# Kernel optimization log

Hardware: AMD Instinct MI355X
Metric: run time of the kernel (lower is better)

The kernel has to match this reference:

```python
import jax, jax.numpy as jnp
import numpy as np
from jax import lax

B, T, MEL, D, H, NC = 8, 256, 128, 192, 4, 20
C_EVENT, C_SCENE = 8, 64
ETA, LR, ALPHA = 0.9, 0.1, 0.01  # memory momentum, write lr, forget rate
EPS = 1e-5


def _ln(x, g, b):
    m = x.mean(-1, keepdims=True)
    v = ((x - m) ** 2).mean(-1, keepdims=True)
    return (x - m) / jnp.sqrt(v + EPS) * g + b


def _mem_step(x, t, M, S, Wk, Wv, Wq, chunk):
    # x: [B,D]; M,S: [B,D,D]. Titans-style neural memory, updated every `chunk` steps.
    k = x @ Wk
    v = x @ Wv
    q = x @ Wq
    err = v - jnp.einsum('bd,bde->be', k, M)          # surprise / prediction error
    S_new = ETA * S + LR * jnp.einsum('bd,be->bde', k, err)
    M_new = (1.0 - ALPHA) * M + S_new
    upd = (t % chunk) == 0
    S = jnp.where(upd, S_new, S)
    M = jnp.where(upd, M_new, M)
    out = jnp.einsum('bd,bde->be', q, M)              # retrieval
    return out, M, S


def setup_inputs() -> dict:
    key = jax.random.key(0)
    ks = jax.random.split(key, 24)
    w = lambda k, shp, s=0.05: jax.random.normal(k, shp, dtype=jnp.float32) * s
    inp = {
        'x': jax.random.normal(ks[0], (B, T, MEL), dtype=jnp.float32),
        'W_in': w(ks[1], (MEL, D)), 'b_in': jnp.zeros((D,), jnp.float32),
        # MHA at seq_len=1: softmax over one key -> weight 1, so only V and out proj matter
        'Wv_a': w(ks[2], (D, D)), 'bv_a': jnp.zeros((D,), jnp.float32),
        'Wo_a': w(ks[3], (D, D)), 'bo_a': jnp.zeros((D,), jnp.float32),
        # conformer conv module (degenerate seq_len=1: depthwise conv -> center tap)
        'ln1_g': jnp.ones((D,), jnp.float32), 'ln1_b': jnp.zeros((D,), jnp.float32),
        'pw1_w': w(ks[4], (D, 2 * D)), 'pw1_b': jnp.zeros((2 * D,), jnp.float32),
        'dw_w': w(ks[5], (D,), 0.2), 'dw_b': jnp.zeros((D,), jnp.float32),
        'bn_s': jnp.ones((D,), jnp.float32), 'bn_b': jnp.zeros((D,), jnp.float32),
        'pw2_w': w(ks[6], (D, D)), 'pw2_b': jnp.zeros((D,), jnp.float32),
        # theta (event) / delta (scene) neural memory projections
        'Wk_t': w(ks[7], (D, D)), 'Wv_t': w(ks[8], (D, D)), 'Wq_t': w(ks[9], (D, D)),
        'Wk_d': w(ks[10], (D, D)), 'Wv_d': w(ks[11], (D, D)), 'Wq_d': w(ks[12], (D, D)),
        'ln2_g': jnp.ones((D,), jnp.float32), 'ln2_b': jnp.zeros((D,), jnp.float32),
        'Wc': w(ks[13], (D, NC)), 'bc': jnp.zeros((NC,), jnp.float32),
    }
    return inp


def reference(x, W_in, b_in, Wv_a, bv_a, Wo_a, bo_a, ln1_g, ln1_b, pw1_w, pw1_b,
              dw_w, dw_b, bn_s, bn_b, pw2_w, pw2_b, Wk_t, Wv_t, Wq_t,
              Wk_d, Wv_d, Wq_d, ln2_g, ln2_b, Wc, bc):
    xp = x @ W_in + b_in                               # [B,T,D]

    def step(carry, inp):
        x_t, t = inp                                   # x_t: [B,D]
        Mt, St, Md, Sd = carry
        d_out, Md, Sd = _mem_step(x_t, t, Md, Sd, Wk_d, Wv_d, Wq_d, C_SCENE)
        x1 = x_t + 0.5 * d_out
        attn = (x1 @ Wv_a + bv_a) @ Wo_a + bo_a        # single-token self-attn
        x2 = x1 + attn
        h = _ln(x2, ln1_g, ln1_b)
        h = h @ pw1_w + pw1_b
        a, g = jnp.split(h, 2, axis=-1)
        h = a * jax.nn.sigmoid(g)                      # GLU
        h = h * dw_w + dw_b                            # depthwise conv center tap
        h = h * bn_s + bn_b                            # eval-mode BN
        h = jax.nn.silu(h)
        h = h @ pw2_w + pw2_b
        x3 = x2 + h
        t_out, Mt, St = _mem_step(x3, t, Mt, St, Wk_t, Wv_t, Wq_t, C_EVENT)
        x4 = x3 + 0.5 * t_out
        return (Mt, St, Md, Sd), _ln(x4, ln2_g, ln2_b)

    z = jnp.zeros((B, D, D), jnp.float32)
    xs = (jnp.swapaxes(xp, 0, 1), jnp.arange(T))       # [T,B,D], [T]
    _, ys = lax.scan(step, (z, z, z, z), xs)
    y = jnp.swapaxes(ys, 0, 1)                         # [B,T,D]
    pooled = y.mean(axis=1)
    return pooled @ Wc + bc                            # [B,NC]
```

## Files before the change

### kernel.cpp

```cpp
#include <hip/hip_runtime.h>
#include <math.h>

#define Bb 8
#define Tt 256
#define MEL 128
#define Dd 192
#define NCc 20
#define ND 4
#define NT 32
#define ETAc 0.9f
#define LRc 0.1f
#define MDEC 0.99f
#define EPSc 1e-5f
#define PT 4
#define RTT 8
#define PADD 196
#define UPAD 193

__device__ __forceinline__ float sigmoidf_(float x) {
    return 1.0f / (1.0f + __expf(-x));
}

__device__ __forceinline__ float memcoef(int n, int i) {
    float m = LRc, pw = LRc;
    for (int nn = i + 1; nn <= n; nn++) { pw *= ETAc; m = MDEC * m + pw; }
    return m;
}

__device__ __forceinline__ float dot4(float4 a, float4 b) {
    return a.x * b.x + a.y * b.y + a.z * b.z + a.w * b.w;
}

__global__ __launch_bounds__(192) void setup(
    const float* __restrict__ Wv_a, const float* __restrict__ Wo_a,
    const float* __restrict__ bv_a, const float* __restrict__ bo_a,
    const float* __restrict__ Wq_t, const float* __restrict__ Wq_d,
    const float* __restrict__ x, const float* __restrict__ W_in,
    const float* __restrict__ b_in, const float* __restrict__ Wk_d,
    const float* __restrict__ Wv_d,
    float* __restrict__ Wavo_ws, float* __restrict__ b_avo,
    float* __restrict__ WqtT, float* __restrict__ WqdT,
    float* __restrict__ Kd_ws, float* __restrict__ Vd_ws,
    float* __restrict__ pooled, unsigned int* __restrict__ ctr)
{
    __shared__ __align__(16) float smem[512];
    int blk = blockIdx.x, tid = threadIdx.x;

    if (blk < 192) {
        int m = blk;
        smem[tid] = Wv_a[m * Dd + tid];
        __syncthreads();
        int o = tid;
        float acc = 0.f;
        #pragma unroll 8
        for (int k = 0; k < Dd; k += 4) {
            acc += Wo_a[(k + 0) * Dd + o] * smem[k + 0];
            acc += Wo_a[(k + 1) * Dd + o] * smem[k + 1];
            acc += Wo_a[(k + 2) * Dd + o] * smem[k + 2];
            acc += Wo_a[(k + 3) * Dd + o] * smem[k + 3];
        }
        Wavo_ws[m * Dd + o] = acc;
        return;
    }
    if (blk == 192) {
        int o = tid;
        float s = bo_a[o];
        #pragma unroll 4
        for (int m = 0; m < Dd; m++) s += bv_a[m] * Wo_a[m * Dd + o];
        b_avo[o] = s;
        return;
    }
    if (blk < 241) {
        int r0 = 4 * (blk - 193);
        float4 v;
        v.x = Wq_t[(r0 + 0) * Dd + tid];
        v.y = Wq_t[(r0 + 1) * Dd + tid];
        v.z = Wq_t[(r0 + 2) * Dd + tid];
        v.w = Wq_t[(r0 + 3) * Dd + tid];
        *(float4*)&WqtT[tid * Dd + r0] = v;
        return;
    }
    if (blk < 289) {
        int r0 = 4 * (blk - 241);
        float4 v;
        v.x = Wq_d[(r0 + 0) * Dd + tid];
        v.y = Wq_d[(r0 + 1) * Dd + tid];
        v.z = Wq_d[(r0 + 2) * Dd + tid];
        v.w = Wq_d[(r0 + 3) * Dd + tid];
        *(float4*)&WqdT[tid * Dd + r0] = v;
        return;
    }
    if (blk == 289) {
        for (int q = tid; q < Bb * Dd; q += 192) pooled[q] = 0.f;
        if (tid == 0) *ctr = 0u;
        return;
    }

    int q = blk - 290;
    int b = q >> 2, i = q & 3;
    float* XR = smem;
    float* XP = smem + 128;
    if (tid < 128) XR[tid] = x[((size_t)b * Tt + 64 * i) * MEL + tid];
    __syncthreads();
    {
        int o = tid;
        float acc = b_in[o];
        #pragma unroll 8
        for (int k = 0; k < MEL; k += 4) {
            acc += W_in[(k + 0) * Dd + o] * XR[k + 0];
            acc += W_in[(k + 1) * Dd + o] * XR[k + 1];
            acc += W_in[(k + 2) * Dd + o] * XR[k + 2];
            acc += W_in[(k + 3) * Dd + o] * XR[k + 3];
        }
        XP[o] = acc;
    }
    __syncthreads();
    {
        int o = tid;
        float ak = 0.f, av = 0.f;
        #pragma unroll 4
        for (int k = 0; k < Dd; k += 4) {
            float x0 = XP[k + 0], x1 = XP[k + 1], x2 = XP[k + 2], x3 = XP[k + 3];
            ak += Wk_d[(k + 0) * Dd + o] * x0 + Wk_d[(k + 1) * Dd + o] * x1
                + Wk_d[(k + 2) * Dd + o] * x2 + Wk_d[(k + 3) * Dd + o] * x3;
            av += Wv_d[(k + 0) * Dd + o] * x0 + Wv_d[(k + 1) * Dd + o] * x1
                + Wv_d[(k + 2) * Dd + o] * x2 + Wv_d[(k + 3) * Dd + o] * x3;
        }
        Kd_ws[(b * ND + i) * Dd + o] = ak;
        Vd_ws[(b * ND + i) * Dd + o] = av;
    }
}

__global__ __launch_bounds__(192) void delta_solve(
    const float* __restrict__ WqdT, const float* __restrict__ Kd_ws,
    float* __restrict__ Vd_ws, float* __restrict__ Ud_ws)
{
    int blk = blockIdx.x, b = blk / 5, role = blk % 5, tid = threadIdx.x;
    if (role == 0) {
        __shared__ __align__(16) float K4[ND][Dd], V4[ND][Dd];
        __shared__ float G[16], mc[16];
        for (int q = tid; q < ND * 48; q += 192) {
            int i = q / 48, c = q - i * 48;
            ((float4*)K4[i])[c] = ((const float4*)&Kd_ws[(b * ND + i) * Dd])[c];
            ((float4*)V4[i])[c] = ((const float4*)&Vd_ws[(b * ND + i) * Dd])[c];
        }
        __syncthreads();
        if (tid < 16) {
            int i = tid >> 2, j = tid & 3;
            float s = 0.f;
            for (int d = 0; d < Dd; d++) s += K4[i][d] * K4[j][d];
            G[tid] = s;
            mc[tid] = (j <= i) ? memcoef(i, j) : 0.f;
        }
        __syncthreads();
        for (int i = 1; i < ND; i++) {
            float acc = V4[i][tid];
            for (int m = 0; m < i; m++)
                acc -= mc[(i - 1) * ND + m] * G[i * ND + m] * V4[m][tid];
            V4[i][tid] = acc;
        }
        for (int i = 0; i < ND; i++) Vd_ws[(b * ND + i) * Dd + tid] = V4[i][tid];
    } else {
        __shared__ float KS[Dd];
        int i = role - 1;
        KS[tid] = Kd_ws[(b * ND + i) * Dd + tid];
        __syncthreads();
        int o = tid;
        float acc = 0.f;
        #pragma unroll 8
        for (int k = 0; k < Dd; k += 4) {
            acc += WqdT[(k + 0) * Dd + o] * KS[k + 0];
            acc += WqdT[(k + 1) * Dd + o] * KS[k + 1];
            acc += WqdT[(k + 2) * Dd + o] * KS[k + 2];
            acc += WqdT[(k + 3) * Dd + o] * KS[k + 3];
        }
        Ud_ws[(b * ND + i) * Dd + o] = acc;
    }
}

__global__ __launch_bounds__(192) void pipeline(
    const float* __restrict__ x, const float* __restrict__ W_in,
    const float* __restrict__ b_in,
    const float* __restrict__ ln1_g, const float* __restrict__ ln1_b,
    const float* __restrict__ pw1_w, const float* __restrict__ pw1_b,
    const float* __restrict__ dw_w, const float* __restrict__ dw_b,
    const float* __restrict__ bn_s, const float* __restrict__ bn_b,
    const float* __restrict__ pw2_w, const float* __restrict__ pw2_b,
    const float* __restrict__ Wavo_ws, const float* __restrict__ b_avo,
    const float* __restrict__ Ed_ws, const float* __restrict__ Ud_ws,
    const float* __restrict__ Wk_t, const float* __restrict__ Wv_t,
    const float* __restrict__ WqtT,
    float* __restrict__ x3_ws, float* __restrict__ Kt_ws,
    float* __restrict__ Vt_ws, float* __restrict__ Ut_ws)
{
    int blk = blockIdx.x;
    int b = blk >> 6, tile = blk & 63;
    int t0 = tile * PT, n = tile >> 4;
    int tid = threadIdx.x;

    __shared__ __align__(16) float XR[PT][MEL];
    __shared__ __align__(16) float XP[PT][Dd];
    __shared__ __align__(16) float ED[ND][PADD], UD[ND][PADD];
    __shared__ __align__(16) float X1[PT][Dd], X2[PT][Dd];
    __shared__ __align__(16) float LNX[PT][Dd], HG[PT][Dd];
    __shared__ float X3row[Dd];
    __shared__ float KTs[Dd];
    __shared__ float WQs[PT * ND];
    __shared__ float mv[PT][2];

    if (tid < 128) {
        int r = tid >> 5, c = tid & 31;
        ((float4*)XR[r])[c] = ((const float4*)&x[((size_t)b * Tt + t0 + r) * MEL])[c];
    }
    for (int q = tid; q < ND * 48 * 2; q += 192) {
        int which = q >= ND * 48;
        int qq = which ? q - ND * 48 : q;
        int i = qq / 48, c = qq - i * 48;
        if (!which) ((float4*)ED[i])[c] = ((const float4*)&Ed_ws[(b * ND + i) * Dd])[c];
        else        ((float4*)UD[i])[c] = ((const float4*)&Ud_ws[(b * ND + i) * Dd])[c];
    }
    __syncthreads();

    int o = tid;
    {
        float acc[PT];
        float bb = b_in[o];
        #pragma unroll
        for (int r = 0; r < PT; r++) acc[r] = bb;
        #pragma unroll 8
        for (int k = 0; k < MEL; k += 4) {
            float w0 = W_in[(k + 0) * Dd + o], w1 = W_in[(k + 1) * Dd + o];
            float w2 = W_in[(k + 2) * Dd + o], w3 = W_in[(k + 3) * Dd + o];
            #pragma unroll
            for (int r = 0; r < PT; r++) {
                float4 xv = *(const float4*)&XR[r][k];
                acc[r] += w0 * xv.x + w1 * xv.y + w2 * xv.z + w3 * xv.w;
            }
        }
        #pragma unroll
        for (int r = 0; r < PT; r++) XP[r][tid] = acc[r];
    }
    __syncthreads();

    if (tid < 128) {
        int r = tid >> 5, i = (tid >> 3) & 3, c = tid & 7;
        float s = 0.f;
        const float* xp = XP[r];
        const float* u = UD[i];
        #pragma unroll
        for (int j = 0; j < 24; j++) s += xp[c * 24 + j] * u[c * 24 + j];
        s += __shfl_down(s, 4, 8);
        s += __shfl_down(s, 2, 8);
        s += __shfl_down(s, 1, 8);
        if (c == 0) {
            float coef = (i <= n) ? memcoef(n, i) : 0.f;
            WQs[r * ND + i] = s * coef;
        }
    }
    __syncthreads();

    {
        #pragma unroll
        for (int r = 0; r < PT; r++) {
            float dout = WQs[r * ND + 0] * ED[0][tid] + WQs[r * ND + 1] * ED[1][tid]
                       + WQs[r * ND + 2] * ED[2][tid] + WQs[r * ND + 3] * ED[3][tid];
            X1[r][tid] = XP[r][tid] + 0.5f * dout;
        }
    }
    __syncthreads();

    {
        float acc[PT];
        float bb = b_avo[o];
        #pragma unroll
        for (int r = 0; r < PT; r++) acc[r] = bb;
        #pragma unroll 8
        for (int k = 0; k < Dd; k += 4) {
            float w0 = Wavo_ws[(k + 0) * Dd + o], w1 = Wavo_ws[(k + 1) * Dd + o];
            float w2 = Wavo_ws[(k + 2) * Dd + o], w3 = Wavo_ws[(k + 3) * Dd + o];
            #pragma unroll
            for (int r = 0; r < PT; r++) {
                float4 xv = *(const float4*)&X1[r][k];
                acc[r] += w0 * xv.x + w1 * xv.y + w2 * xv.z + w3 * xv.w;
            }
        }
        #pragma unroll
        for (int r = 0; r < PT; r++) X2[r][tid] = X1[r][tid] + acc[r];
    }
    __syncthreads();

    if (tid < 128) {
        int r = tid >> 5, j = tid & 31;
        float s = 0.f, sq = 0.f;
        for (int d = j; d < Dd; d += 32) { float v = X2[r][d]; s += v; sq += v * v; }
        for (int off = 16; off > 0; off >>= 1) {
            s += __shfl_down(s, off, 32); sq += __shfl_down(sq, off, 32);
        }
        if (j == 0) {
            float mean = s / Dd;
            mv[r][0] = mean;
            mv[r][1] = rsqrtf(sq / Dd - mean * mean + EPSc);
        }
    }
    __syncthreads();
    {
        float g = ln1_g[tid], bb = ln1_b[tid];
        #pragma unroll
        for (int r = 0; r < PT; r++)
            LNX[r][tid] = (X2[r][tid] - mv[r][0]) * mv[r][1] * g + bb;
    }
    __syncthreads();

    {
        float aa[PT], gg[PT];
        float ba = pw1_b[o], bg = pw1_b[o + Dd];
        #pragma unroll
        for (int r = 0; r < PT; r++) { aa[r] = ba; gg[r] = bg; }
        #pragma unroll 4
        for (int k = 0; k < Dd; k += 4) {
            float wa0 = pw1_w[(k + 0) * 2 * Dd + o], wg0 = pw1_w[(k + 0) * 2 * Dd + Dd + o];
            float wa1 = pw1_w[(k + 1) * 2 * Dd + o], wg1 = pw1_w[(k + 1) * 2 * Dd + Dd + o];
            float wa2 = pw1_w[(k + 2) * 2 * Dd + o], wg2 = pw1_w[(k + 2) * 2 * Dd + Dd + o];
            float wa3 = pw1_w[(k + 3) * 2 * Dd + o], wg3 = pw1_w[(k + 3) * 2 * Dd + Dd + o];
            #pragma unroll
            for (int r = 0; r < PT; r++) {
                float4 xv = *(const float4*)&LNX[r][k];
                aa[r] += wa0 * xv.x + wa1 * xv.y + wa2 * xv.z + wa3 * xv.w;
                gg[r] += wg0 * xv.x + wg1 * xv.y + wg2 * xv.z + wg3 * xv.w;
            }
        }
        float dww = dw_w[o], dwb = dw_b[o], bns = bn_s[o], bnb = bn_b[o];
        #pragma unroll
        for (int r = 0; r < PT; r++) {
            float h = aa[r] * sigmoidf_(gg[r]);
            h = h * dww + dwb;
            h = h * bns + bnb;
            h = h * sigmoidf_(h);
            HG[r][tid] = h;
        }
    }
    __syncthreads();

    {
        float acc[PT];
        float bb = pw2_b[o];
        #pragma unroll
        for (int r = 0; r < PT; r++) acc[r] = bb;
        #pragma unroll 8
        for (int k = 0; k < Dd; k += 4) {
            float w0 = pw2_w[(k + 0) * Dd + o], w1 = pw2_w[(k + 1) * Dd + o];
            float w2 = pw2_w[(k + 2) * Dd + o], w3 = pw2_w[(k + 3) * Dd + o];
            #pragma unroll
            for (int r = 0; r < PT; r++) {
                float4 xv = *(const float4*)&HG[r][k];
                acc[r] += w0 * xv.x + w1 * xv.y + w2 * xv.z + w3 * xv.w;
            }
        }
        #pragma unroll
        for (int r = 0; r < PT; r++) {
            float v = X2[r][tid] + acc[r];
            if (r == 0) X3row[tid] = v;
            x3_ws[((size_t)b * Tt + t0 + r) * Dd + tid] = v;
        }
    }

    if ((tile & 1) == 0) {
        int i8 = tile >> 1;
        __syncthreads();
        {
            float ak = 0.f, av = 0.f;
            #pragma unroll 4
            for (int k = 0; k < Dd; k += 4) {
                float x0 = X3row[k + 0], x1v = X3row[k + 1];
                float x2v = X3row[k + 2], x3v = X3row[k + 3];
                ak += Wk_t[(k + 0) * Dd + o] * x0 + Wk_t[(k + 1) * Dd + o] * x1v
                    + Wk_t[(k + 2) * Dd + o] * x2v + Wk_t[(k + 3) * Dd + o] * x3v;
                av += Wv_t[(k + 0) * Dd + o] * x0 + Wv_t[(k + 1) * Dd + o] * x1v
                    + Wv_t[(k + 2) * Dd + o] * x2v + Wv_t[(k + 3) * Dd + o] * x3v;
            }
            Kt_ws[(b * NT + i8) * Dd + o] = ak;
            Vt_ws[(b * NT + i8) * Dd + o] = av;
            KTs[o] = ak;
        }
        __syncthreads();
        {
            float au = 0.f;
            #pragma unroll 8
            for (int k = 0; k < Dd; k += 4) {
                au += WqtT[(k + 0) * Dd + o] * KTs[k + 0]
                    + WqtT[(k + 1) * Dd + o] * KTs[k + 1]
                    + WqtT[(k + 2) * Dd + o] * KTs[k + 2]
                    + WqtT[(k + 3) * Dd + o] * KTs[k + 3];
            }
            Ut_ws[(b * NT + i8) * Dd + o] = au;
        }
    }
}

__global__ __launch_bounds__(192) void theta_solve(
    const float* __restrict__ Kt_ws, const float* __restrict__ Vt_ws,
    float* __restrict__ Et_ws)
{
    int b = blockIdx.x, tid = threadIdx.x;
    __shared__ __align__(16) float K[NT][PADD], V[NT][PADD];
    __shared__ float G[NT * NT], mcc[NT * NT];
    __shared__ float T[NT * 33];

    for (int q = tid; q < NT * 48; q += 192) {
        int i = q / 48, c = q - i * 48;
        ((float4*)K[i])[c] = ((const float4*)&Kt_ws[(b * NT + i) * Dd])[c];
        ((float4*)V[i])[c] = ((const float4*)&Vt_ws[(b * NT + i) * Dd])[c];
    }
    if (tid < NT) {
        int i = tid;
        float m = 0.f, pw = LRc;
        for (int nn = 0; nn < NT; nn++) {
            float v;
            if (nn < i) v = 0.f;
            else if (nn == i) { m = LRc; v = m; }
            else { pw *= ETAc; m = MDEC * m + pw; v = m; }
            mcc[nn * NT + i] = v;
        }
    }
    __syncthreads();
    for (int p = tid; p < NT * NT; p += 192) {
        int i = p >> 5, j = p & 31;
        const float4* ki = (const float4*)K[i];
        const float4* kj = (const float4*)K[j];
        float s = 0.f;
        #pragma unroll 4
        for (int kk = 0; kk < 48; kk++) s += dot4(ki[kk], kj[kk]);
        G[p] = s;
    }
    __syncthreads();
    for (int p = tid; p < NT * NT; p += 192) {
        int i = p >> 5, m = p & 31;
        G[p] = (m < i) ? mcc[(i - 1) * NT + m] * G[p] : 0.f;
    }
    __syncthreads();
    if (tid < NT) {
        int j = tid;
        T[j * 33 + j] = 1.f;
        for (int i = j + 1; i < NT; i++) {
            float s = 0.f;
            for (int m = j; m < i; m++) s += G[i * NT + m] * T[m * 33 + j];
            T[i * 33 + j] = -s;
        }
    }
    __syncthreads();
    {
        for (int i = 0; i < NT; i++) {
            float s = 0.f;
            for (int j = 0; j <= i; j++) s += T[i * 33 + j] * V[j][tid];
            Et_ws[(b * NT + i) * Dd + tid] = s;
        }
    }
}

__global__ __launch_bounds__(256) void retrieve(
    const float* __restrict__ x3_ws, const float* __restrict__ Ut_ws,
    const float* __restrict__ Et_ws, const float* __restrict__ ln2_g,
    const float* __restrict__ ln2_b, float* __restrict__ pooled,
    const float* __restrict__ Wc, const float* __restrict__ bc,
    float* __restrict__ out, unsigned int* __restrict__ ctr)
{
    int blk = blockIdx.x, b = blk >> 5, tile = blk & 31;
    int t0 = tile * RTT, n = tile;
    int tid = threadIdx.x;

    __shared__ float UT[NT][UPAD];
    __shared__ __align__(16) float XS[RTT][PADD];
    __shared__ float WQ[RTT * NT];
    __shared__ float mv[RTT][2];
    __shared__ float PLD[Bb * Dd];
    __shared__ bool isLast;

    for (int q = tid; q < NT * Dd; q += 256) {
        int i = q / Dd, c = q - i * Dd;
        UT[i][c] = Ut_ws[(size_t)b * NT * Dd + q];
    }
    for (int q = tid; q < RTT * 48; q += 256) {
        int r = q / 48, c = q - r * 48;
        ((float4*)XS[r])[c] = ((const float4*)&x3_ws[((size_t)b * Tt + t0 + r) * Dd])[c];
    }
    __syncthreads();

    {
        int r = tid >> 5, i = tid & 31;
        const float* u = UT[i];
        const float* xr = XS[r];
        float s = 0.f;
        #pragma unroll 8
        for (int kk = 0; kk < Dd; kk++) s += u[kk] * xr[kk];
        float coef = (i <= n) ? memcoef(n, i) : 0.f;
        WQ[tid] = s * coef;
    }
    __syncthreads();

    if (tid < Dd) {
        float acc[RTT] = {};
        #pragma unroll 4
        for (int i = 0; i < NT; i++) {
            float e = Et_ws[(b * NT + i) * Dd + tid];
            #pragma unroll
            for (int r = 0; r < RTT; r++) acc[r] += WQ[r * NT + i] * e;
        }
        #pragma unroll
        for (int r = 0; r < RTT; r++) XS[r][tid] += 0.5f * acc[r];
    }
    __syncthreads();

    {
        int r = tid >> 5, j = tid & 31;
        float s = 0.f, sq = 0.f;
        for (int d = j; d < Dd; d += 32) { float v = XS[r][d]; s += v; sq += v * v; }
        for (int off = 16; off > 0; off >>= 1) {
            s += __shfl_down(s, off, 32); sq += __shfl_down(sq, off, 32);
        }
        if (j == 0) {
            float mean = s / Dd;
            mv[r][0] = mean;
            mv[r][1] = rsqrtf(sq / Dd - mean * mean + EPSc);
        }
    }
    __syncthreads();

    if (tid < Dd) {
        float g = ln2_g[tid], bb = ln2_b[tid];
        float sum = 0.f;
        #pragma unroll
        for (int r = 0; r < RTT; r++)
            sum += (XS[r][tid] - mv[r][0]) * mv[r][1] * g + bb;
        atomicAdd(&pooled[b * Dd + tid], sum);
    }

    __threadfence();
    if (tid == 0) {
        unsigned int old = atomicAdd(ctr, 1u);
        isLast = (old == (unsigned)(Bb * 32 - 1));
    }
    __syncthreads();
    if (isLast) {
        __threadfence();
        for (int q = tid; q < Bb * Dd; q += 256)
            PLD[q] = *(volatile const float*)&pooled[q];
        __syncthreads();
        if (tid < Bb * NCc) {
            int bo = tid / NCc, c = tid - bo * NCc;
            float s = 0.f;
            for (int d = 0; d < Dd; d++) s += PLD[bo * Dd + d] * Wc[d * NCc + c];
            out[tid] = s * (1.0f / Tt) + bc[c];
        }
    }
}

extern "C" void kernel_launch(void* const* d_in, const int* in_sizes, int n_in,
                              void* d_out, int out_size, void* d_ws, size_t ws_size,
                              hipStream_t stream) {
    const float* x     = (const float*)d_in[0];
    const float* W_in  = (const float*)d_in[1];
    const float* b_in  = (const float*)d_in[2];
    const float* Wv_a  = (const float*)d_in[3];
    const float* bv_a  = (const float*)d_in[4];
    const float* Wo_a  = (const float*)d_in[5];
    const float* bo_a  = (const float*)d_in[6];
    const float* ln1_g = (const float*)d_in[7];
    const float* ln1_b = (const float*)d_in[8];
    const float* pw1_w = (const float*)d_in[9];
    const float* pw1_b = (const float*)d_in[10];
    const float* dw_w  = (const float*)d_in[11];
    const float* dw_b  = (const float*)d_in[12];
    const float* bn_s  = (const float*)d_in[13];
    const float* bn_b  = (const float*)d_in[14];
    const float* pw2_w = (const float*)d_in[15];
    const float* pw2_b = (const float*)d_in[16];
    const float* Wk_t  = (const float*)d_in[17];
    const float* Wv_t  = (const float*)d_in[18];
    const float* Wq_t  = (const float*)d_in[19];
    const float* Wk_d  = (const float*)d_in[20];
    const float* Wv_d  = (const float*)d_in[21];
    const float* Wq_d  = (const float*)d_in[22];
    const float* ln2_g = (const float*)d_in[23];
    const float* ln2_b = (const float*)d_in[24];
    const float* Wc    = (const float*)d_in[25];
    const float* bc    = (const float*)d_in[26];

    float* ws = (float*)d_ws;
    size_t off = 0;
    float* x3_ws   = ws + off; off += (size_t)Bb * Tt * Dd;
    float* Kd_ws   = ws + off; off += Bb * ND * Dd;
    float* Vd_ws   = ws + off; off += Bb * ND * Dd;
    float* Ud_ws   = ws + off; off += Bb * ND * Dd;
    float* Kt_ws   = ws + off; off += Bb * NT * Dd;
    float* Vt_ws   = ws + off; off += Bb * NT * Dd;
    float* Et_ws   = ws + off; off += Bb * NT * Dd;
    float* Ut_ws   = ws + off; off += Bb * NT * Dd;
    float* pooled  = ws + off; off += Bb * Dd;
    float* Wavo_ws = ws + off; off += Dd * Dd;
    float* WqtT    = ws + off; off += Dd * Dd;
    float* WqdT    = ws + off; off += Dd * Dd;
    float* b_avo   = ws + off; off += Dd;
    unsigned int* ctr = (unsigned int*)(ws + off); off += 1;

    setup<<<322, 192, 0, stream>>>(
        Wv_a, Wo_a, bv_a, bo_a, Wq_t, Wq_d,
        x, W_in, b_in, Wk_d, Wv_d,
        Wavo_ws, b_avo, WqtT, WqdT, Kd_ws, Vd_ws, pooled, ctr);
    delta_solve<<<Bb * 5, 192, 0, stream>>>(WqdT, Kd_ws, Vd_ws, Ud_ws);
    pipeline<<<Bb * 64, 192, 0, stream>>>(
        x, W_in, b_in, ln1_g, ln1_b, pw1_w, pw1_b, dw_w, dw_b,
        bn_s, bn_b, pw2_w, pw2_b, Wavo_ws, b_avo, Vd_ws, Ud_ws,
        Wk_t, Wv_t, WqtT, x3_ws, Kt_ws, Vt_ws, Ut_ws);
    theta_solve<<<Bb, 192, 0, stream>>>(Kt_ws, Vt_ws, Et_ws);
    retrieve<<<Bb * 32, 256, 0, stream>>>(
        x3_ws, Ut_ws, Et_ws, ln2_g, ln2_b, pooled, Wc, bc, (float*)d_out, ctr);
}
```

Baseline: 224.7 us.

## Fuse all stages into one cooperative persistent kernel with grid syncs

Replaces the five separate kernel launches with a single cooperative kernel that runs each phase in a grid-stride loop, separated by grid.sync(). The pipeline is also split into finer phases (separate theta-solve stages and a final classifier phase), all sharing one LDS union. The aim is to remove launch gaps and the atomic last-block counter. In exchange it adds grid-wide barrier costs, forces a 256-thread block shape where only 192 threads work in many phases, and reduces occupancy because the LDS union is sized for the largest phase.

```diff
diff --git a/kernel.cpp b/kernel.cpp
--- a/kernel.cpp
+++ b/kernel.cpp
@@ -1,5 +1,8 @@
 #include <hip/hip_runtime.h>
+#include <hip/hip_cooperative_groups.h>
 #include <math.h>
+
+namespace cg = cooperative_groups;
 
 #define Bb 8
 #define Tt 256
@@ -16,6 +19,13 @@
 #define RTT 8
 #define PADD 196
 #define UPAD 193
+#define BLK_THR 256
+#define NA 322
+#define NB 40
+#define NC_ 512
+#define NDp 256
+#define NE 8
+#define NF 256
 
 __device__ __forceinline__ float sigmoidf_(float x) {
     return 1.0f / (1.0f + __expf(-x));
@@ -31,222 +41,211 @@
     return a.x * b.x + a.y * b.y + a.z * b.z + a.w * b.w;
 }
 
-__global__ __launch_bounds__(192) void setup(
-    const float* __restrict__ Wv_a, const float* __restrict__ Wo_a,
-    const float* __restrict__ bv_a, const float* __restrict__ bo_a,
-    const float* __restrict__ Wq_t, const float* __restrict__ Wq_d,
-    const float* __restrict__ x, const float* __restrict__ W_in,
-    const float* __restrict__ b_in, const float* __restrict__ Wk_d,
-    const float* __restrict__ Wv_d,
-    float* __restrict__ Wavo_ws, float* __restrict__ b_avo,
-    float* __restrict__ WqtT, float* __restrict__ WqdT,
-    float* __restrict__ Kd_ws, float* __restrict__ Vd_ws,
-    float* __restrict__ pooled, unsigned int* __restrict__ ctr)
-{
-    __shared__ __align__(16) float smem[512];
-    int blk = blockIdx.x, tid = threadIdx.x;
-
+struct CoopArgs {
+    const float *x, *W_in, *b_in, *Wv_a, *bv_a, *Wo_a, *bo_a;
+    const float *ln1_g, *ln1_b, *pw1_w, *pw1_b, *dw_w, *dw_b, *bn_s, *bn_b;
+    const float *pw2_w, *pw2_b, *Wk_t, *Wv_t, *Wq_t, *Wk_d, *Wv_d, *Wq_d;
+    const float *ln2_g, *ln2_b, *Wc, *bc;
+    float *x3_ws, *Kd_ws, *Vd_ws, *Ud_ws, *Kt_ws, *Vt_ws, *Et_ws, *Ut_ws;
+    float *Sg_ws, *pooled, *Wavo_ws, *WqtT, *WqdT, *b_avo, *out;
+};
+
+struct LdsA { float col[Dd]; float XR[MEL]; float XP[Dd]; };
+struct LdsB { float K4[ND][Dd]; float V4[ND][Dd]; float G[16], mc[16]; float KS[Dd]; };
+struct LdsC {
+    float XR[PT][MEL]; float XP[PT][Dd];
+    float ED[ND][PADD], UD[ND][PADD];
+    float X1[PT][Dd], X2[PT][Dd], LNX[PT][Dd], HG[PT][Dd];
+    float WQs[PT * ND]; float mv[PT][2];
+};
+struct LdsD { float XS[Dd]; float KS[Dd]; };
+struct LdsE1 { float K[NT][PADD]; };
+struct LdsE2 { float S[NT * NT]; float T[NT * 33]; };
+struct LdsF { float UT[NT][UPAD]; float XS[RTT][PADD]; float WQ[RTT * NT]; float mv[RTT][2]; };
+struct LdsG { float PLD[Bb * Dd]; };
+
+union LDSU {
+    LdsA a; LdsB b; LdsC c; LdsD d; LdsE1 e1; LdsE2 e2; LdsF f; LdsG g;
+};
+
+__device__ void phaseA(const CoopArgs& a, LdsA& L, int blk, int tid)
+{
     if (blk < 192) {
         int m = blk;
-        smem[tid] = Wv_a[m * Dd + tid];
+        if (tid < Dd) L.col[tid] = a.Wv_a[m * Dd + tid];
         __syncthreads();
-        int o = tid;
-        float acc = 0.f;
-        #pragma unroll 8
-        for (int k = 0; k < Dd; k += 4) {
-            acc += Wo_a[(k + 0) * Dd + o] * smem[k + 0];
-            acc += Wo_a[(k + 1) * Dd + o] * smem[k + 1];
-            acc += Wo_a[(k + 2) * Dd + o] * smem[k + 2];
-            acc += Wo_a[(k + 3) * Dd + o] * smem[k + 3];
-        }
-        Wavo_ws[m * Dd + o] = acc;
-        return;
-    }
-    if (blk == 192) {
-        int o = tid;
-        float s = bo_a[o];
-        #pragma unroll 4
-        for (int m = 0; m < Dd; m++) s += bv_a[m] * Wo_a[m * Dd + o];
-        b_avo[o] = s;
-        return;
-    }
-    if (blk < 241) {
+        if (tid < Dd) {
+            int o = tid;
+            float acc = 0.f;
+            #pragma unroll 8
+            for (int k = 0; k < Dd; k += 4) {
+                acc += a.Wo_a[(k + 0) * Dd + o] * L.col[k + 0];
+                acc += a.Wo_a[(k + 1) * Dd + o] * L.col[k + 1];
+                acc += a.Wo_a[(k + 2) * Dd + o] * L.col[k + 2];
+                acc += a.Wo_a[(k + 3) * Dd + o] * L.col[k + 3];
+            }
+            a.Wavo_ws[m * Dd + o] = acc;
+        }
+    } else if (blk == 192) {
+        if (tid < Dd) {
+            int o = tid;
+            float s = a.bo_a[o];
+            #pragma unroll 4
+            for (int m = 0; m < Dd; m++) s += a.bv_a[m] * a.Wo_a[m * Dd + o];
+            a.b_avo[o] = s;
+        }
+    } else if (blk < 241) {
         int r0 = 4 * (blk - 193);
-        float4 v;
-        v.x = Wq_t[(r0 + 0) * Dd + tid];
-        v.y = Wq_t[(r0 + 1) * Dd + tid];
-        v.z = Wq_t[(r0 + 2) * Dd + tid];
-        v.w = Wq_t[(r0 + 3) * Dd + tid];
-        *(float4*)&WqtT[tid * Dd + r0] = v;
-        return;
-    }
-    if (blk < 289) {
+        if (tid < Dd) {
+            float4 v;
+            v.x = a.Wq_t[(r0 + 0) * Dd + tid];
+            v.y = a.Wq_t[(r0 + 1) * Dd + tid];
+            v.z = a.Wq_t[(r0 + 2) * Dd + tid];
+            v.w = a.Wq_t[(r0 + 3) * Dd + tid];
+            *(float4*)&a.WqtT[tid * Dd + r0] = v;
+        }
+    } else if (blk < 289) {
         int r0 = 4 * (blk - 241);
-        float4 v;
-        v.x = Wq_d[(r0 + 0) * Dd + tid];
-        v.y = Wq_d[(r0 + 1) * Dd + tid];
-        v.z = Wq_d[(r0 + 2) * Dd + tid];
-        v.w = Wq_d[(r0 + 3) * Dd + tid];
-        *(float4*)&WqdT[tid * Dd + r0] = v;
-        return;
-    }
-    if (blk == 289) {
-        for (int q = tid; q < Bb * Dd; q += 192) pooled[q] = 0.f;
-        if (tid == 0) *ctr = 0u;
-        return;
-    }
-
-    int q = blk - 290;
-    int b = q >> 2, i = q & 3;
-    float* XR = smem;
-    float* XP = smem + 128;
-    if (tid < 128) XR[tid] = x[((size_t)b * Tt + 64 * i) * MEL + tid];
-    __syncthreads();
-    {
-        int o = tid;
-        float acc = b_in[o];
-        #pragma unroll 8
-        for (int k = 0; k < MEL; k += 4) {
-            acc += W_in[(k + 0) * Dd + o] * XR[k + 0];
-            acc += W_in[(k + 1) * Dd + o] * XR[k + 1];
-            acc += W_in[(k + 2) * Dd + o] * XR[k + 2];
-            acc += W_in[(k + 3) * Dd + o] * XR[k + 3];
-        }
-        XP[o] = acc;
-    }
-    __syncthreads();
-    {
-        int o = tid;
-        float ak = 0.f, av = 0.f;
-        #pragma unroll 4
-        for (int k = 0; k < Dd; k += 4) {
-            float x0 = XP[k + 0], x1 = XP[k + 1], x2 = XP[k + 2], x3 = XP[k + 3];
-            ak += Wk_d[(k + 0) * Dd + o] * x0 + Wk_d[(k + 1) * Dd + o] * x1
-                + Wk_d[(k + 2) * Dd + o] * x2 + Wk_d[(k + 3) * Dd + o] * x3;
-            av += Wv_d[(k + 0) * Dd + o] * x0 + Wv_d[(k + 1) * Dd + o] * x1
-                + Wv_d[(k + 2) * Dd + o] * x2 + Wv_d[(k + 3) * Dd + o] * x3;
-        }
-        Kd_ws[(b * ND + i) * Dd + o] = ak;
-        Vd_ws[(b * ND + i) * Dd + o] = av;
-    }
-}
-
-__global__ __launch_bounds__(192) void delta_solve(
-    const float* __restrict__ WqdT, const float* __restrict__ Kd_ws,
-    float* __restrict__ Vd_ws, float* __restrict__ Ud_ws)
-{
-    int blk = blockIdx.x, b = blk / 5, role = blk % 5, tid = threadIdx.x;
+        if (tid < Dd) {
+            float4 v;
+            v.x = a.Wq_d[(r0 + 0) * Dd + tid];
+            v.y = a.Wq_d[(r0 + 1) * Dd + tid];
+            v.z = a.Wq_d[(r0 + 2) * Dd + tid];
+            v.w = a.Wq_d[(r0 + 3) * Dd + tid];
+            *(float4*)&a.WqdT[tid * Dd + r0] = v;
+        }
+    } else if (blk == 289) {
+        for (int q = tid; q < Bb * Dd; q += BLK_THR) a.pooled[q] = 0.f;
+    } else if (blk < 322) {
+        int q = blk - 290;
+        int b = q >> 2, i = q & 3;
+        if (tid < 128) L.XR[tid] = a.x[((size_t)b * Tt + 64 * i) * MEL + tid];
+        __syncthreads();
+        if (tid < Dd) {
+            int o = tid;
+            float acc = a.b_in[o];
+            #pragma unroll 8
+            for (int k = 0; k < MEL; k += 4) {
+                acc += a.W_in[(k + 0) * Dd + o] * L.XR[k + 0];
+                acc += a.W_in[(k + 1) * Dd + o] * L.XR[k + 1];
+                acc += a.W_in[(k + 2) * Dd + o] * L.XR[k + 2];
+                acc += a.W_in[(k + 3) * Dd + o] * L.XR[k + 3];
+            }
+            L.XP[o] = acc;
+        }
+        __syncthreads();
+        if (tid < Dd) {
+            int o = tid;
+            float ak = 0.f, av = 0.f;
+            #pragma unroll 4
+            for (int k = 0; k < Dd; k += 4) {
+                float x0 = L.XP[k + 0], x1 = L.XP[k + 1];
+                float x2 = L.XP[k + 2], x3 = L.XP[k + 3];
+                ak += a.Wk_d[(k + 0) * Dd + o] * x0 + a.Wk_d[(k + 1) * Dd + o] * x1
+                    + a.Wk_d[(k + 2) * Dd + o] * x2 + a.Wk_d[(k + 3) * Dd + o] * x3;
+                av += a.Wv_d[(k + 0) * Dd + o] * x0 + a.Wv_d[(k + 1) * Dd + o] * x1
+                    + a.Wv_d[(k + 2) * Dd + o] * x2 + a.Wv_d[(k + 3) * Dd + o] * x3;
+            }
+            a.Kd_ws[(b * ND + i) * Dd + o] = ak;
+            a.Vd_ws[(b * ND + i) * Dd + o] = av;
+        }
+    }
+    __syncthreads();
+}
+
+__device__ void phaseB(const CoopArgs& a, LdsB& L, int blk, int tid)
+{
+    int b = blk / 5, role = blk % 5;
     if (role == 0) {
-        __shared__ __align__(16) float K4[ND][Dd], V4[ND][Dd];
-        __shared__ float G[16], mc[16];
-        for (int q = tid; q < ND * 48; q += 192) {
-            int i = q / 48, c = q - i * 48;
-            ((float4*)K4[i])[c] = ((const float4*)&Kd_ws[(b * ND + i) * Dd])[c];
-            ((float4*)V4[i])[c] = ((const float4*)&Vd_ws[(b * ND + i) * Dd])[c];
+        for (int q = tid; q < ND * Dd; q += BLK_THR) {
+            int i = q / Dd, c = q - i * Dd;
+            L.K4[i][c] = a.Kd_ws[(size_t)b * ND * Dd + q];
+            L.V4[i][c] = a.Vd_ws[(size_t)b * ND * Dd + q];
         }
         __syncthreads();
         if (tid < 16) {
             int i = tid >> 2, j = tid & 3;
             float s = 0.f;
-            for (int d = 0; d < Dd; d++) s += K4[i][d] * K4[j][d];
-            G[tid] = s;
-            mc[tid] = (j <= i) ? memcoef(i, j) : 0.f;
+            for (int d = 0; d < Dd; d++) s += L.K4[i][d] * L.K4[j][d];
+            L.G[tid] = s;
+            L.mc[tid] = (j <= i) ? memcoef(i, j) : 0.f;
         }
         __syncthreads();
-        for (int i = 1; i < ND; i++) {
-            float acc = V4[i][tid];
-            for (int m = 0; m < i; m++)
-                acc -= mc[(i - 1) * ND + m] * G[i * ND + m] * V4[m][tid];
-            V4[i][tid] = acc;
-        }
-        for (int i = 0; i < ND; i++) Vd_ws[(b * ND + i) * Dd + tid] = V4[i][tid];
+        if (tid < Dd) {
+            for (int i = 1; i < ND; i++) {
+                float acc = L.V4[i][tid];
+                for (int m = 0; m < i; m++)
+                    acc -= L.mc[(i - 1) * ND + m] * L.G[i * ND + m] * L.V4[m][tid];
+                L.V4[i][tid] = acc;
+            }
+            for (int i = 0; i < ND; i++)
+                a.Vd_ws[(b * ND + i) * Dd + tid] = L.V4[i][tid];
+        }
     } else {
-        __shared__ float KS[Dd];
         int i = role - 1;
-        KS[tid] = Kd_ws[(b * ND + i) * Dd + tid];
+        if (tid < Dd) L.KS[tid] = a.Kd_ws[(b * ND + i) * Dd + tid];
         __syncthreads();
-        int o = tid;
-        float acc = 0.f;
-        #pragma unroll 8
-        for (int k = 0; k < Dd; k += 4) {
-            acc += WqdT[(k + 0) * Dd + o] * KS[k + 0];
-            acc += WqdT[(k + 1) * Dd + o] * KS[k + 1];
-            acc += WqdT[(k + 2) * Dd + o] * KS[k + 2];
-            acc += WqdT[(k + 3) * Dd + o] * KS[k + 3];
-        }
-        Ud_ws[(b * ND + i) * Dd + o] = acc;
-    }
-}
-
-__global__ __launch_bounds__(192) void pipeline(
-    const float* __restrict__ x, const float* __restrict__ W_in,
-    const float* __restrict__ b_in,
-    const float* __restrict__ ln1_g, const float* __restrict__ ln1_b,
-    const float* __restrict__ pw1_w, const float* __restrict__ pw1_b,
-    const float* __restrict__ dw_w, const float* __restrict__ dw_b,
-    const float* __restrict__ bn_s, const float* __restrict__ bn_b,
-    const float* __restrict__ pw2_w, const float* __restrict__ pw2_b,
-    const float* __restrict__ Wavo_ws, const float* __restrict__ b_avo,
-    const float* __restrict__ Ed_ws, const float* __restrict__ Ud_ws,
-    const float* __restrict__ Wk_t, const float* __restrict__ Wv_t,
-    const float* __restrict__ WqtT,
-    float* __restrict__ x3_ws, float* __restrict__ Kt_ws,
-    float* __restrict__ Vt_ws, float* __restrict__ Ut_ws)
-{
-    int blk = blockIdx.x;
+        if (tid < Dd) {
+            int o = tid;
+            float acc = 0.f;
+            #pragma unroll 8
+            for (int k = 0; k < Dd; k += 4) {
+                acc += a.WqdT[(k + 0) * Dd + o] * L.KS[k + 0];
+                acc += a.WqdT[(k + 1) * Dd + o] * L.KS[k + 1];
+                acc += a.WqdT[(k + 2) * Dd + o] * L.KS[k + 2];
+                acc += a.WqdT[(k + 3) * Dd + o] * L.KS[k + 3];
+            }
+            a.Ud_ws[(b * ND + i) * Dd + o] = acc;
+        }
+    }
+    __syncthreads();
+}
+
+__device__ void phaseC(const CoopArgs& a, LdsC& L, int blk, int tid)
+{
     int b = blk >> 6, tile = blk & 63;
     int t0 = tile * PT, n = tile >> 4;
-    int tid = threadIdx.x;
-
-    __shared__ __align__(16) float XR[PT][MEL];
-    __shared__ __align__(16) float XP[PT][Dd];
-    __shared__ __align__(16) float ED[ND][PADD], UD[ND][PADD];
-    __shared__ __align__(16) float X1[PT][Dd], X2[PT][Dd];
-    __shared__ __align__(16) float LNX[PT][Dd], HG[PT][Dd];
-    __shared__ float X3row[Dd];
-    __shared__ float KTs[Dd];
-    __shared__ float WQs[PT * ND];
-    __shared__ float mv[PT][2];
 
     if (tid < 128) {
         int r = tid >> 5, c = tid & 31;
-        ((float4*)XR[r])[c] = ((const float4*)&x[((size_t)b * Tt + t0 + r) * MEL])[c];
-    }
-    for (int q = tid; q < ND * 48 * 2; q += 192) {
+        ((float4*)L.XR[r])[c] =
+            ((const float4*)&a.x[((size_t)b * Tt + t0 + r) * MEL])[c];
+    }
+    for (int q = tid; q < ND * 48 * 2; q += BLK_THR) {
         int which = q >= ND * 48;
         int qq = which ? q - ND * 48 : q;
         int i = qq / 48, c = qq - i * 48;
-        if (!which) ((float4*)ED[i])[c] = ((const float4*)&Ed_ws[(b * ND + i) * Dd])[c];
-        else        ((float4*)UD[i])[c] = ((const float4*)&Ud_ws[(b * ND + i) * Dd])[c];
+        if (!which) ((float4*)L.ED[i])[c] = ((const float4*)&a.Vd_ws[(b * ND + i) * Dd])[c];
+        else        ((float4*)L.UD[i])[c] = ((const float4*)&a.Ud_ws[(b * ND + i) * Dd])[c];
     }
     __syncthreads();
 
     int o = tid;
-    {
+    if (tid < Dd) {
         float acc[PT];
-        float bb = b_in[o];
+        float bb = a.b_in[o];
         #pragma unroll
         for (int r = 0; r < PT; r++) acc[r] = bb;
         #pragma unroll 8
         for (int k = 0; k < MEL; k += 4) {
-            float w0 = W_in[(k + 0) * Dd + o], w1 = W_in[(k + 1) * Dd + o];
-            float w2 = W_in[(k + 2) * Dd + o], w3 = W_in[(k + 3) * Dd + o];
+            float w0 = a.W_in[(k + 0) * Dd + o], w1 = a.W_in[(k + 1) * Dd + o];
+            float w2 = a.W_in[(k + 2) * Dd + o], w3 = a.W_in[(k + 3) * Dd + o];
             #pragma unroll
             for (int r = 0; r < PT; r++) {
-                float4 xv = *(const float4*)&XR[r][k];
+                float4 xv = *(const float4*)&L.XR[r][k];
                 acc[r] += w0 * xv.x + w1 * xv.y + w2 * xv.z + w3 * xv.w;
             }
         }
         #pragma unroll
-        for (int r = 0; r < PT; r++) XP[r][tid] = acc[r];
+        for (int r = 0; r < PT; r++) L.XP[r][tid] = acc[r];
     }
     __syncthreads();
 
     if (tid < 128) {
         int r = tid >> 5, i = (tid >> 3) & 3, c = tid & 7;
         float s = 0.f;
-        const float* xp = XP[r];
-        const float* u = UD[i];
+        const float* xp = L.XP[r];
+        const float* u = L.UD[i];
         #pragma unroll
         for (int j = 0; j < 24; j++) s += xp[c * 24 + j] * u[c * 24 + j];
         s += __shfl_down(s, 4, 8);
@@ -254,246 +253,236 @@
         s += __shfl_down(s, 1, 8);
         if (c == 0) {
             float coef = (i <= n) ? memcoef(n, i) : 0.f;
-            WQs[r * ND + i] = s * coef;
-        }
-    }
-    __syncthreads();
-
-    {
+            L.WQs[r * ND + i] = s * coef;
+        }
+    }
+    __syncthreads();
+
+    if (tid < Dd) {
         #pragma unroll
         for (int r = 0; r < PT; r++) {
-            float dout = WQs[r * ND + 0] * ED[0][tid] + WQs[r * ND + 1] * ED[1][tid]
-                       + WQs[r * ND + 2] * ED[2][tid] + WQs[r * ND + 3] * ED[3][tid];
-            X1[r][tid] = XP[r][tid] + 0.5f * dout;
-        }
-    }
-    __syncthreads();
-
-    {
+            float dout = L.WQs[r * ND + 0] * L.ED[0][tid]
+                       + L.WQs[r * ND + 1] * L.ED[1][tid]
+                       + L.WQs[r * ND + 2] * L.ED[2][tid]
+                       + L.WQs[r * ND + 3] * L.ED[3][tid];
+            L.X1[r][tid] = L.XP[r][tid] + 0.5f * dout;
+        }
+    }
+    __syncthreads();
+
+    if (tid < Dd) {
         float acc[PT];
-        float bb = b_avo[o];
+        float bb = a.b_avo[o];
         #pragma unroll
         for (int r = 0; r < PT; r++) acc[r] = bb;
         #pragma unroll 8
         for (int k = 0; k < Dd; k += 4) {
-            float w0 = Wavo_ws[(k + 0) * Dd + o], w1 = Wavo_ws[(k + 1) * Dd + o];
-            float w2 = Wavo_ws[(k + 2) * Dd + o], w3 = Wavo_ws[(k + 3) * Dd + o];
+            float w0 = a.Wavo_ws[(k + 0) * Dd + o], w1 = a.Wavo_ws[(k + 1) * Dd + o];
+            float w2 = a.Wavo_ws[(k + 2) * Dd + o], w3 = a.Wavo_ws[(k + 3) * Dd + o];
             #pragma unroll
             for (int r = 0; r < PT; r++) {
-                float4 xv = *(const float4*)&X1[r][k];
+                float4 xv = *(const float4*)&L.X1[r][k];
                 acc[r] += w0 * xv.x + w1 * xv.y + w2 * xv.z + w3 * xv.w;
             }
         }
         #pragma unroll
-        for (int r = 0; r < PT; r++) X2[r][tid] = X1[r][tid] + acc[r];
+        for (int r = 0; r < PT; r++) L.X2[r][tid] = L.X1[r][tid] + acc[r];
     }
     __syncthreads();
 
     if (tid < 128) {
         int r = tid >> 5, j = tid & 31;
         float s = 0.f, sq = 0.f;
-        for (int d = j; d < Dd; d += 32) { float v = X2[r][d]; s += v; sq += v * v; }
+        for (int d = j; d < Dd; d += 32) { float v = L.X2[r][d]; s += v; sq += v * v; }
         for (int off = 16; off > 0; off >>= 1) {
             s += __shfl_down(s, off, 32); sq += __shfl_down(sq, off, 32);
         }
         if (j == 0) {
             float mean = s / Dd;
-            mv[r][0] = mean;
-            mv[r][1] = rsqrtf(sq / Dd - mean * mean + EPSc);
-        }
-    }
-    __syncthreads();
-    {
-        float g = ln1_g[tid], bb = ln1_b[tid];
+            L.mv[r][0] = mean;
+            L.mv[r][1] = rsqrtf(sq / Dd - mean * mean + EPSc);
+        }
+    }
+    __syncthreads();
+    if (tid < Dd) {
+        float g = a.ln1_g[tid], bb = a.ln1_b[tid];
         #pragma unroll
         for (int r = 0; r < PT; r++)
-            LNX[r][tid] = (X2[r][tid] - mv[r][0]) * mv[r][1] * g + bb;
-    }
-    __syncthreads();
-
-    {
+            L.LNX[r][tid] = (L.X2[r][tid] - L.mv[r][0]) * L.mv[r][1] * g + bb;
+    }
+    __syncthreads();
+
+    if (tid < Dd) {
         float aa[PT], gg[PT];
-        float ba = pw1_b[o], bg = pw1_b[o + Dd];
+        float ba = a.pw1_b[o], bg = a.pw1_b[o + Dd];
         #pragma unroll
         for (int r = 0; r < PT; r++) { aa[r] = ba; gg[r] = bg; }
         #pragma unroll 4
         for (int k = 0; k < Dd; k += 4) {
-            float wa0 = pw1_w[(k + 0) * 2 * Dd + o], wg0 = pw1_w[(k + 0) * 2 * Dd + Dd + o];
-            float wa1 = pw1_w[(k + 1) * 2 * Dd + o], wg1 = pw1_w[(k + 1) * 2 * Dd + Dd + o];
-            float wa2 = pw1_w[(k + 2) * 2 * Dd + o], wg2 = pw1_w[(k + 2) * 2 * Dd + Dd + o];
-            float wa3 = pw1_w[(k + 3) * 2 * Dd + o], wg3 = pw1_w[(k + 3) * 2 * Dd + Dd + o];
+            float wa0 = a.pw1_w[(k + 0) * 2 * Dd + o], wg0 = a.pw1_w[(k + 0) * 2 * Dd + Dd + o];
+            float wa1 = a.pw1_w[(k + 1) * 2 * Dd + o], wg1 = a.pw1_w[(k + 1) * 2 * Dd + Dd + o];
+            float wa2 = a.pw1_w[(k + 2) * 2 * Dd + o], wg2 = a.pw1_w[(k + 2) * 2 * Dd + Dd + o];
+            float wa3 = a.pw1_w[(k + 3) * 2 * Dd + o], wg3 = a.pw1_w[(k + 3) * 2 * Dd + Dd + o];
             #pragma unroll
             for (int r = 0; r < PT; r++) {
-                float4 xv = *(const float4*)&LNX[r][k];
+                float4 xv = *(const float4*)&L.LNX[r][k];
                 aa[r] += wa0 * xv.x + wa1 * xv.y + wa2 * xv.z + wa3 * xv.w;
                 gg[r] += wg0 * xv.x + wg1 * xv.y + wg2 * xv.z + wg3 * xv.w;
             }
         }
-        float dww = dw_w[o], dwb = dw_b[o], bns = bn_s[o], bnb = bn_b[o];
+        float dww = a.dw_w[o], dwb = a.dw_b[o], bns = a.bn_s[o], bnb = a.bn_b[o];
         #pragma unroll
         for (int r = 0; r < PT; r++) {
             float h = aa[r] * sigmoidf_(gg[r]);
             h = h * dww + dwb;
             h = h * bns + bnb;
             h = h * sigmoidf_(h);
-            HG[r][tid] = h;
-        }
-    }
-    __syncthreads();
-
-    {
+            L.HG[r][tid] = h;
+        }
+    }
+    __syncthreads();
+
+    if (tid < Dd) {
         float acc[PT];
-        float bb = pw2_b[o];
+        float bb = a.pw2_b[o];
         #pragma unroll
         for (int r = 0; r < PT; r++) acc[r] = bb;
         #pragma unroll 8
         for (int k = 0; k < Dd; k += 4) {
-            float w0 = pw2_w[(k + 0) * Dd + o], w1 = pw2_w[(k + 1) * Dd + o];
-            float w2 = pw2_w[(k + 2) * Dd + o], w3 = pw2_w[(k + 3) * Dd + o];
+            float w0 = a.pw2_w[(k + 0) * Dd + o], w1 = a.pw2_w[(k + 1) * Dd + o];
+            float w2 = a.pw2_w[(k + 2) * Dd + o], w3 = a.pw2_w[(k + 3) * Dd + o];
             #pragma unroll
             for (int r = 0; r < PT; r++) {
-                float4 xv = *(const float4*)&HG[r][k];
+                float4 xv = *(const float4*)&L.HG[r][k];
                 acc[r] += w0 * xv.x + w1 * xv.y + w2 * xv.z + w3 * xv.w;
             }
         }
         #pragma unroll
-        for (int r = 0; r < PT; r++) {
-            float v = X2[r][tid] + acc[r];
-            if (r == 0) X3row[tid] = v;
-            x3_ws[((size_t)b * Tt + t0 + r) * Dd + tid] = v;
-        }
-    }
-
-    if ((tile & 1) == 0) {
-        int i8 = tile >> 1;
-        __syncthreads();
-        {
-            float ak = 0.f, av = 0.f;
+        for (int r = 0; r < PT; r++)
+            a.x3_ws[((size_t)b * Tt + t0 + r) * Dd + tid] = L.X2[r][tid] + acc[r];
+    }
+    __syncthreads();
+}
+
+__device__ void phaseD(const CoopArgs& a, LdsD& L, int blk, int tid)
+{
+    int b = blk >> 5, i = blk & 31;
+    if (tid < Dd) L.XS[tid] = a.x3_ws[((size_t)b * Tt + 8 * i) * Dd + tid];
+    __syncthreads();
+    if (tid < Dd) {
+        int o = tid;
+        float ak = 0.f, av = 0.f;
+        #pragma unroll 4
+        for (int k = 0; k < Dd; k += 4) {
+            float x0 = L.XS[k + 0], x1 = L.XS[k + 1];
+            float x2 = L.XS[k + 2], x3 = L.XS[k + 3];
+            ak += a.Wk_t[(k + 0) * Dd + o] * x0 + a.Wk_t[(k + 1) * Dd + o] * x1
+                + a.Wk_t[(k + 2) * Dd + o] * x2 + a.Wk_t[(k + 3) * Dd + o] * x3;
+            av += a.Wv_t[(k + 0) * Dd + o] * x0 + a.Wv_t[(k + 1) * Dd + o] * x1
+                + a.Wv_t[(k + 2) * Dd + o] * x2 + a.Wv_t[(k + 3) * Dd + o] * x3;
+        }
+        a.Kt_ws[(b * NT + i) * Dd + o] = ak;
+        a.Vt_ws[(b * NT + i) * Dd + o] = av;
+        L.KS[o] = ak;
+    }
+    __syncthreads();
+    if (tid < Dd) {
+        int o = tid;
+        float au = 0.f;
+        #pragma unroll 8
+        for (int k = 0; k < Dd; k += 4) {
+            au += a.WqtT[(k + 0) * Dd + o] * L.KS[k + 0]
+                + a.WqtT[(k + 1) * Dd + o] * L.KS[k + 1]
+                + a.WqtT[(k + 2) * Dd + o] * L.KS[k + 2]
+                + a.WqtT[(k + 3) * Dd + o] * L.KS[k + 3];
+        }
+        a.Ut_ws[(b * NT + i) * Dd + o] = au;
+    }
+    __syncthreads();
+}
+
+__device__ void phaseE1(const CoopArgs& a, LdsE1& L, int blk, int tid)
+{
+    int b = blk;
+    for (int q = tid; q < NT * 48; q += BLK_THR) {
+        int i = q / 48, c = q - i * 48;
+        ((float4*)L.K[i])[c] = ((const float4*)&a.Kt_ws[(b * NT + i) * Dd])[c];
+    }
+    __syncthreads();
+    for (int p = tid; p < NT * NT; p += BLK_THR) {
+        int i = p >> 5, m = p & 31;
+        float sv = 0.f;
+        if (m < i) {
+            const float4* ki = (const float4*)L.K[i];
+            const float4* km = (const float4*)L.K[m];
+            float s = 0.f;
             #pragma unroll 4
-            for (int k = 0; k < Dd; k += 4) {
-                float x0 = X3row[k + 0], x1v = X3row[k + 1];
-                float x2v = X3row[k + 2], x3v = X3row[k + 3];
-                ak += Wk_t[(k + 0) * Dd + o] * x0 + Wk_t[(k + 1) * Dd + o] * x1v
-                    + Wk_t[(k + 2) * Dd + o] * x2v + Wk_t[(k + 3) * Dd + o] * x3v;
-                av += Wv_t[(k + 0) * Dd + o] * x0 + Wv_t[(k + 1) * Dd + o] * x1v
-                    + Wv_t[(k + 2) * Dd + o] * x2v + Wv_t[(k + 3) * Dd + o] * x3v;
-            }
-            Kt_ws[(b * NT + i8) * Dd + o] = ak;
-            Vt_ws[(b * NT + i8) * Dd + o] = av;
-            KTs[o] = ak;
-        }
-        __syncthreads();
-        {
-            float au = 0.f;
-            #pragma unroll 8
-            for (int k = 0; k < Dd; k += 4) {
-                au += WqtT[(k + 0) * Dd + o] * KTs[k + 0]
-                    + WqtT[(k + 1) * Dd + o] * KTs[k + 1]
-                    + WqtT[(k + 2) * Dd + o] * KTs[k + 2]
-                    + WqtT[(k + 3) * Dd + o] * KTs[k + 3];
-            }
-            Ut_ws[(b * NT + i8) * Dd + o] = au;
-        }
-    }
-}
-
-__global__ __launch_bounds__(192) void theta_solve(
-    const float* __restrict__ Kt_ws, const float* __restrict__ Vt_ws,
-    float* __restrict__ Et_ws)
-{
-    int b = blockIdx.x, tid = threadIdx.x;
-    __shared__ __align__(16) float K[NT][PADD], V[NT][PADD];
-    __shared__ float G[NT * NT], mcc[NT * NT];
-    __shared__ float T[NT * 33];
-
-    for (int q = tid; q < NT * 48; q += 192) {
-        int i = q / 48, c = q - i * 48;
-        ((float4*)K[i])[c] = ((const float4*)&Kt_ws[(b * NT + i) * Dd])[c];
-        ((float4*)V[i])[c] = ((const float4*)&Vt_ws[(b * NT + i) * Dd])[c];
-    }
-    if (tid < NT) {
-        int i = tid;
-        float m = 0.f, pw = LRc;
-        for (int nn = 0; nn < NT; nn++) {
-            float v;
-            if (nn < i) v = 0.f;
-            else if (nn == i) { m = LRc; v = m; }
-            else { pw *= ETAc; m = MDEC * m + pw; v = m; }
-            mcc[nn * NT + i] = v;
-        }
-    }
-    __syncthreads();
-    for (int p = tid; p < NT * NT; p += 192) {
-        int i = p >> 5, j = p & 31;
-        const float4* ki = (const float4*)K[i];
-        const float4* kj = (const float4*)K[j];
-        float s = 0.f;
-        #pragma unroll 4
-        for (int kk = 0; kk < 48; kk++) s += dot4(ki[kk], kj[kk]);
-        G[p] = s;
-    }
-    __syncthreads();
-    for (int p = tid; p < NT * NT; p += 192) {
-        int i = p >> 5, m = p & 31;
-        G[p] = (m < i) ? mcc[(i - 1) * NT + m] * G[p] : 0.f;
-    }
+            for (int kk = 0; kk < 48; kk++) s += dot4(ki[kk], km[kk]);
+            sv = memcoef(i - 1, m) * s;
+        }
+        a.Sg_ws[(size_t)b * NT * NT + p] = sv;
+    }
+    __syncthreads();
+}
+
+__device__ void phaseE2(const CoopArgs& a, LdsE2& L, int blk, int tid)
+{
+    int b = blk;
+    for (int p = tid; p < NT * NT; p += BLK_THR)
+        L.S[p] = a.Sg_ws[(size_t)b * NT * NT + p];
     __syncthreads();
     if (tid < NT) {
         int j = tid;
-        T[j * 33 + j] = 1.f;
+        L.T[j * 33 + j] = 1.f;
         for (int i = j + 1; i < NT; i++) {
             float s = 0.f;
-            for (int m = j; m < i; m++) s += G[i * NT + m] * T[m * 33 + j];
-            T[i * 33 + j] = -s;
-        }
-    }
-    __syncthreads();
-    {
-        for (int i = 0; i < NT; i++) {
-            float s = 0.f;
-            for (int j = 0; j <= i; j++) s += T[i * 33 + j] * V[j][tid];
-            Et_ws[(b * NT + i) * Dd + tid] = s;
-        }
-    }
-}
-
-__global__ __launch_bounds__(256) void retrieve(
-    const float* __restrict__ x3_ws, const float* __restrict__ Ut_ws,
-    const float* __restrict__ Et_ws, const float* __restrict__ ln2_g,
-    const float* __restrict__ ln2_b, float* __restrict__ pooled,
-    const float* __restrict__ Wc, const float* __restrict__ bc,
-    float* __restrict__ out, unsigned int* __restrict__ ctr)
-{
-    int blk = blockIdx.x, b = blk >> 5, tile = blk & 31;
+            for (int m = j; m < i; m++) s += L.S[i * NT + m] * L.T[m * 33 + j];
+            L.T[i * 33 + j] = -s;
+        }
+    }
+    __syncthreads();
+    if (tid < Dd) {
+        float accv[NT];
+        #pragma unroll
+        for (int i = 0; i < NT; i++) accv[i] = 0.f;
+        #pragma unroll
+        for (int j = 0; j < NT; j++) {
+            float v = a.Vt_ws[(b * NT + j) * Dd + tid];
+            #pragma unroll
+            for (int i = 0; i < NT; i++)
+                if (i >= j) accv[i] += L.T[i * 33 + j] * v;
+        }
+        for (int i = 0; i < NT; i++)
+            a.Et_ws[(b * NT + i) * Dd + tid] = accv[i];
+    }
+    __syncthreads();
+}
+
+__device__ void phaseF(const CoopArgs& a, LdsF& L, int blk, int tid)
+{
+    int b = blk >> 5, tile = blk & 31;
     int t0 = tile * RTT, n = tile;
-    int tid = threadIdx.x;
-
-    __shared__ float UT[NT][UPAD];
-    __shared__ __align__(16) float XS[RTT][PADD];
-    __shared__ float WQ[RTT * NT];
-    __shared__ float mv[RTT][2];
-    __shared__ float PLD[Bb * Dd];
-    __shared__ bool isLast;
-
-    for (int q = tid; q < NT * Dd; q += 256) {
+
+    for (int q = tid; q < NT * Dd; q += BLK_THR) {
         int i = q / Dd, c = q - i * Dd;
-        UT[i][c] = Ut_ws[(size_t)b * NT * Dd + q];
-    }
-    for (int q = tid; q < RTT * 48; q += 256) {
+        L.UT[i][c] = a.Ut_ws[(size_t)b * NT * Dd + q];
+    }
+    for (int q = tid; q < RTT * 48; q += BLK_THR) {
         int r = q / 48, c = q - r * 48;
-        ((float4*)XS[r])[c] = ((const float4*)&x3_ws[((size_t)b * Tt + t0 + r) * Dd])[c];
+        ((float4*)L.XS[r])[c] =
+            ((const float4*)&a.x3_ws[((size_t)b * Tt + t0 + r) * Dd])[c];
     }
     __syncthreads();
 
     {
         int r = tid >> 5, i = tid & 31;
-        const float* u = UT[i];
-        const float* xr = XS[r];
+        const float* u = L.UT[i];
+        const float* xr = L.XS[r];
         float s = 0.f;
         #pragma unroll 8
         for (int kk = 0; kk < Dd; kk++) s += u[kk] * xr[kk];
         float coef = (i <= n) ? memcoef(n, i) : 0.f;
-        WQ[tid] = s * coef;
+        L.WQ[tid] = s * coef;
     }
     __syncthreads();
 
@@ -501,90 +490,89 @@
         float acc[RTT] = {};
         #pragma unroll 4
         for (int i = 0; i < NT; i++) {
-            float e = Et_ws[(b * NT + i) * Dd + tid];
+            float e = a.Et_ws[(b * NT + i) * Dd + tid];
             #pragma unroll
-            for (int r = 0; r < RTT; r++) acc[r] += WQ[r * NT + i] * e;
-        }
-        #pragma unroll
-        for (int r = 0; r < RTT; r++) XS[r][tid] += 0.5f * acc[r];
+            for (int r = 0; r < RTT; r++) acc[r] += L.WQ[r * NT + i] * e;
+        }
+        #pragma unroll
+        for (int r = 0; r < RTT; r++) L.XS[r][tid] += 0.5f * acc[r];
     }
     __syncthreads();
 
     {
         int r = tid >> 5, j = tid & 31;
         float s = 0.f, sq = 0.f;
-        for (int d = j; d < Dd; d += 32) { float v = XS[r][d]; s += v; sq += v * v; }
+        for (int d = j; d < Dd; d += 32) { float v = L.XS[r][d]; s += v; sq += v * v; }
         for (int off = 16; off > 0; off >>= 1) {
             s += __shfl_down(s, off, 32); sq += __shfl_down(sq, off, 32);
         }
         if (j == 0) {
             float mean = s / Dd;
-            mv[r][0] = mean;
-            mv[r][1] = rsqrtf(sq / Dd - mean * mean + EPSc);
-        }
-    }
-    __syncthreads();
-
-    if (tid < Dd) {
-        float g = ln2_g[tid], bb = ln2_b[tid];
+            L.mv[r][0] = mean;
+            L.mv[r][1] = rsqrtf(sq / Dd - mean * mean + EPSc);
+        }
+    }
+    __syncthreads();
+
+    if (tid < Dd) {
+        float g = a.ln2_g[tid], bb = a.ln2_b[tid];
         float sum = 0.f;
         #pragma unroll
         for (int r = 0; r < RTT; r++)
-            sum += (XS[r][tid] - mv[r][0]) * mv[r][1] * g + bb;
-        atomicAdd(&pooled[b * Dd + tid], sum);
-    }
-
-    __threadfence();
-    if (tid == 0) {
-        unsigned int old = atomicAdd(ctr, 1u);
-        isLast = (old == (unsigned)(Bb * 32 - 1));
-    }
-    __syncthreads();
-    if (isLast) {
-        __threadfence();
-        for (int q = tid; q < Bb * Dd; q += 256)
-            PLD[q] = *(volatile const float*)&pooled[q];
-        __syncthreads();
-        if (tid < Bb * NCc) {
-            int bo = tid / NCc, c = tid - bo * NCc;
-            float s = 0.f;
-            for (int d = 0; d < Dd; d++) s += PLD[bo * Dd + d] * Wc[d * NCc + c];
-            out[tid] = s * (1.0f / Tt) + bc[c];
-        }
-    }
-}
+            sum += (L.XS[r][tid] - L.mv[r][0]) * L.mv[r][1] * g + bb;
+        atomicAdd(&a.pooled[b * Dd + tid], sum);
+    }
+    __syncthreads();
+}
+
+__device__ void phaseG(const CoopArgs& a, LdsG& L, int tid)
+{
+    for (int q = tid; q < Bb * Dd; q += BLK_THR) L.PLD[q] = a.pooled[q];
+    __syncthreads();
+    if (tid < Bb * NCc) {
+        int bo = tid / NCc, c = tid - bo * NCc;
+        float s = 0.f;
+        for (int d = 0; d < Dd; d++) s += L.PLD[bo * Dd + d] * a.Wc[d * NCc + c];
+        a.out[tid] = s * (1.0f / Tt) + a.bc[c];
+    }
+    __syncthreads();
+}
+
+__global__ __launch_bounds__(BLK_THR, 2) void fused(CoopArgs a)
+{
+    cg::grid_group grid = cg::this_grid();
+    __shared__ LDSU U;
+    int tid = threadIdx.x;
+
+    for (int vb = blockIdx.x; vb < NA; vb += gridDim.x) phaseA(a, U.a, vb, tid);
+    grid.sync();
+    for (int vb = blockIdx.x; vb < NB; vb += gridDim.x) phaseB(a, U.b, vb, tid);
+    grid.sync();
+    for (int vb = blockIdx.x; vb < NC_; vb += gridDim.x) phaseC(a, U.c, vb, tid);
+    grid.sync();
+    for (int vb = blockIdx.x; vb < NDp; vb += gridDim.x) phaseD(a, U.d, vb, tid);
+    grid.sync();
+    for (int vb = blockIdx.x; vb < NE; vb += gridDim.x) phaseE1(a, U.e1, vb, tid);
+    grid.sync();
+    for (int vb = blockIdx.x; vb < NE; vb += gridDim.x) phaseE2(a, U.e2, vb, tid);
+    grid.sync();
+    for (int vb = blockIdx.x; vb < NF; vb += gridDim.x) phaseF(a, U.f, vb, tid);
+    grid.sync();
+    if (blockIdx.x == 0) phaseG(a, U.g, tid);
+}
+
+__global__ __launch_bounds__(BLK_THR) void kA(CoopArgs a) { __shared__ LdsA L; phaseA(a, L, blockIdx.x, threadIdx.x); }
+__global__ __launch_bounds__(BLK_THR) void kB(CoopArgs a) { __shared__ LdsB L; phaseB(a, L, blockIdx.x, threadIdx.x); }
+__global__ __launch_bounds__(BLK_THR) void kC(CoopArgs a) { __shared__ LdsC L; phaseC(a, L, blockIdx.x, threadIdx.x); }
+__global__ __launch_bounds__(BLK_THR) void kD(CoopArgs a) { __shared__ LdsD L; phaseD(a, L, blockIdx.x, threadIdx.x); }
+__global__ __launch_bounds__(BLK_THR) void kE1(CoopArgs a){ __shared__ LdsE1 L; phaseE1(a, L, blockIdx.x, threadIdx.x); }
+__global__ __launch_bounds__(BLK_THR) void kE2(CoopArgs a){ __shared__ LdsE2 L; phaseE2(a, L, blockIdx.x, threadIdx.x); }
+__global__ __launch_bounds__(BLK_THR) void kF(CoopArgs a) { __shared__ LdsF L; phaseF(a, L, blockIdx.x, threadIdx.x); }
+__global__ __launch_bounds__(BLK_THR) void kG(CoopArgs a) { __shared__ LdsG L; phaseG(a, L, threadIdx.x); }
 
 extern "C" void kernel_launch(void* const* d_in, const int* in_sizes, int n_in,
                               void* d_out, int out_size, void* d_ws, size_t ws_size,
                               hipStream_t stream) {
-    const float* x     = (const float*)d_in[0];
-    const float* W_in  = (const float*)d_in[1];
-    const float* b_in  = (const float*)d_in[2];
-    const float* Wv_a  = (const float*)d_in[3];
-    const float* bv_a  = (const float*)d_in[4];
-    const float* Wo_a  = (const float*)d_in[5];
-    const float* bo_a  = (const float*)d_in[6];
-    const float* ln1_g = (const float*)d_in[7];
-    const float* ln1_b = (const float*)d_in[8];
-    const float* pw1_w = (const float*)d_in[9];
-    const float* pw1_b = (const float*)d_in[10];
-    const float* dw_w  = (const float*)d_in[11];
-    const float* dw_b  = (const float*)d_in[12];
-    const float* bn_s  = (const float*)d_in[13];
-    const float* bn_b  = (const float*)d_in[14];
-    const float* pw2_w = (const float*)d_in[15];
-    const float* pw2_b = (const float*)d_in[16];
-    const float* Wk_t  = (const float*)d_in[17];
-    const float* Wv_t  = (const float*)d_in[18];
-    const float* Wq_t  = (const float*)d_in[19];
-    const float* Wk_d  = (const float*)d_in[20];
-    const float* Wv_d  = (const float*)d_in[21];
-    const float* Wq_d  = (const float*)d_in[22];
-    const float* ln2_g = (const float*)d_in[23];
-    const float* ln2_b = (const float*)d_in[24];
-    const float* Wc    = (const float*)d_in[25];
-    const float* bc    = (const float*)d_in[26];
-
     float* ws = (float*)d_ws;
     size_t off = 0;
     float* x3_ws   = ws + off; off += (size_t)Bb * Tt * Dd;
@@ -595,23 +583,71 @@
     float* Vt_ws   = ws + off; off += Bb * NT * Dd;
     float* Et_ws   = ws + off; off += Bb * NT * Dd;
     float* Ut_ws   = ws + off; off += Bb * NT * Dd;
+    float* Sg_ws   = ws + off; off += Bb * NT * NT;
     float* pooled  = ws + off; off += Bb * Dd;
     float* Wavo_ws = ws + off; off += Dd * Dd;
     float* WqtT    = ws + off; off += Dd * Dd;
     float* WqdT    = ws + off; off += Dd * Dd;
     float* b_avo   = ws + off; off += Dd;
-    unsigned int* ctr = (unsigned int*)(ws + off); off += 1;
-
-    setup<<<322, 192, 0, stream>>>(
-        Wv_a, Wo_a, bv_a, bo_a, Wq_t, Wq_d,
-        x, W_in, b_in, Wk_d, Wv_d,
-        Wavo_ws, b_avo, WqtT, WqdT, Kd_ws, Vd_ws, pooled, ctr);
-    delta_solve<<<Bb * 5, 192, 0, stream>>>(WqdT, Kd_ws, Vd_ws, Ud_ws);
-    pipeline<<<Bb * 64, 192, 0, stream>>>(
-        x, W_in, b_in, ln1_g, ln1_b, pw1_w, pw1_b, dw_w, dw_b,
-        bn_s, bn_b, pw2_w, pw2_b, Wavo_ws, b_avo, Vd_ws, Ud_ws,
-        Wk_t, Wv_t, WqtT, x3_ws, Kt_ws, Vt_ws, Ut_ws);
-    theta_solve<<<Bb, 192, 0, stream>>>(Kt_ws, Vt_ws, Et_ws);
-    retrieve<<<Bb * 32, 256, 0, stream>>>(
-        x3_ws, Ut_ws, Et_ws, ln2_g, ln2_b, pooled, Wc, bc, (float*)d_out, ctr);
-}
+
+    CoopArgs a;
+    a.x     = (const float*)d_in[0];
+    a.W_in  = (const float*)d_in[1];
+    a.b_in  = (const float*)d_in[2];
+    a.Wv_a  = (const float*)d_in[3];
+    a.bv_a  = (const float*)d_in[4];
+    a.Wo_a  = (const float*)d_in[5];
+    a.bo_a  = (const float*)d_in[6];
+    a.ln1_g = (const float*)d_in[7];
+    a.ln1_b = (const float*)d_in[8];
+    a.pw1_w = (const float*)d_in[9];
+    a.pw1_b = (const float*)d_in[10];
+    a.dw_w  = (const float*)d_in[11];
+    a.dw_b  = (const float*)d_in[12];
+    a.bn_s  = (const float*)d_in[13];
+    a.bn_b  = (const float*)d_in[14];
+    a.pw2_w = (const float*)d_in[15];
+    a.pw2_b = (const float*)d_in[16];
+    a.Wk_t  = (const float*)d_in[17];
+    a.Wv_t  = (const float*)d_in[18];
+    a.Wq_t  = (const float*)d_in[19];
+    a.Wk_d  = (const float*)d_in[20];
+    a.Wv_d  = (const float*)d_in[21];
+    a.Wq_d  = (const float*)d_in[22];
+    a.ln2_g = (const float*)d_in[23];
+    a.ln2_b = (const float*)d_in[24];
+    a.Wc    = (const float*)d_in[25];
+    a.bc    = (const float*)d_in[26];
+    a.x3_ws = x3_ws;   a.Kd_ws = Kd_ws;  a.Vd_ws = Vd_ws;  a.Ud_ws = Ud_ws;
+    a.Kt_ws = Kt_ws;   a.Vt_ws = Vt_ws;  a.Et_ws = Et_ws;  a.Ut_ws = Ut_ws;
+    a.Sg_ws = Sg_ws;   a.pooled = pooled; a.Wavo_ws = Wavo_ws;
+    a.WqtT = WqtT;     a.WqdT = WqdT;     a.b_avo = b_avo;
+    a.out = (float*)d_out;
+
+    int dev = 0;
+    (void)hipGetDevice(&dev);
+    int numCU = 0;
+    (void)hipDeviceGetAttribute(&numCU, hipDeviceAttributeMultiprocessorCount, dev);
+    int nbPerCU = 0;
+    hipError_t qe = hipOccupancyMaxActiveBlocksPerMultiprocessor(&nbPerCU, fused, BLK_THR, 0);
+
+    bool coop_ok = (qe == hipSuccess) && (numCU > 0) && (nbPerCU > 0)
+                   && ((long)nbPerCU * numCU >= 64);
+    if (coop_ok) {
+        long cap = (long)nbPerCU * numCU;
+        int grid = (int)(cap < NC_ ? cap : NC_);
+        void* kargs[] = { &a };
+        hipError_t le = hipLaunchCooperativeKernel(
+            reinterpret_cast<void*>(fused), dim3(grid), dim3(BLK_THR), kargs, 0, stream);
+        if (le == hipSuccess) return;
+    }
+
+    kA<<<NA, BLK_THR, 0, stream>>>(a);
+    kB<<<NB, BLK_THR, 0, stream>>>(a);
+    kC<<<NC_, BLK_THR, 0, stream>>>(a);
+    kD<<<NDp, BLK_THR, 0, stream>>>(a);
+    kE1<<<NE, BLK_THR, 0, stream>>>(a);
+    kE2<<<NE, BLK_THR, 0, stream>>>(a);
+    kF<<<NF, BLK_THR, 0, stream>>>(a);
+    kG<<<1, BLK_THR, 0, stream>>>(a);
+}
```

New measurement: 497.5 us. +121.4%, slower.
